# Optimization experiments

Hardware: AMD Instinct MI355X
Metric: run time of the kernel (lower is better)

## Reference

```python
import jax, jax.numpy as jnp
import numpy as np

N, C, O, H, S, SHARE = 30000, 128, 128, 8, 16, 8
D = O // H            # mid_planes = 16
OS = O // SHARE       # 16
OFFSETS = [15000, 30000]
EPS = 1e-5


def _knn(p, offsets, k):
    """Exact per-batch KNN (incl. self), chunked to bound memory."""
    n = p.shape[0]
    idx = np.empty((n, k), dtype=np.int64)
    start = 0
    for end in offsets:
        pb = p[start:end]
        sq = (pb * pb).sum(-1)
        for qs in range(0, pb.shape[0], 1024):
            q = pb[qs:qs + 1024]
            d = sq[qs:qs + q.shape[0], None] - 2.0 * (q @ pb.T) + sq[None, :]
            part = np.argpartition(d, k - 1, axis=1)[:, :k]
            idx[start + qs:start + qs + q.shape[0]] = part + start
        start = end
    return idx


def _ln(x, g, b):
    m = x.mean(-1, keepdims=True)
    v = ((x - m) ** 2).mean(-1, keepdims=True)
    return (x - m) / jnp.sqrt(v + EPS) * g + b


def setup_inputs() -> dict:
    rng = np.random.default_rng(0)
    p_np = (rng.standard_normal((N, 3)) * 5.0).astype(np.float32)
    idx = _knn(p_np, OFFSETS, S)

    key = jax.random.key(0)
    ks = jax.random.split(key, 12)

    def lin(k, i, o):
        return (jax.random.normal(k, (i, o), jnp.float32) / np.sqrt(i)).astype(jnp.float32)

    return {
        "p": jnp.asarray(p_np),
        "x": jax.random.normal(ks[0], (N, C), jnp.float32),
        "idx": jnp.asarray(idx),
        "Wq": lin(ks[1], C, O), "bq": jnp.zeros((O,), jnp.float32),
        "Wk": lin(ks[2], C, O), "bk": jnp.zeros((O,), jnp.float32),
        "Wv": lin(ks[3], C, O), "bv": jnp.zeros((O,), jnp.float32),
        "Wp1": lin(ks[4], 3, 3), "bp1": jnp.zeros((3,), jnp.float32),
        "gp": jnp.ones((3,), jnp.float32), "betap": jnp.zeros((3,), jnp.float32),
        "Wp2": lin(ks[5], 3, O), "bp2": jnp.zeros((O,), jnp.float32),
        "gw1": jnp.ones((D,), jnp.float32), "betaw1": jnp.zeros((D,), jnp.float32),
        "Ww1": lin(ks[6], D, OS), "bw1": jnp.zeros((OS,), jnp.float32),
        "gw2": jnp.ones((OS,), jnp.float32), "betaw2": jnp.zeros((OS,), jnp.float32),
        "Ww2": lin(ks[7], OS, OS), "bw2": jnp.zeros((OS,), jnp.float32),
    }


def reference(p, x, idx, Wq, bq, Wk, bk, Wv, bv, Wp1, bp1, gp, betap, Wp2, bp2,
              gw1, betaw1, Ww1, bw1, gw2, betaw2, Ww2, bw2):
    xq = (x @ Wq + bq).reshape(N, H, D)          # (N,H,D)
    xk = x @ Wk + bk                              # (N,O)
    xv = x @ Wv + bv
    kg = xk[idx].reshape(N, S, H, D)              # neighbor gather
    vg = xv[idx].reshape(N, S, H, D)
    pr = p[idx] - p[:, None, :]                   # relative coords (N,S,3)
    pe = jax.nn.relu(_ln(pr @ Wp1 + bp1, gp, betap)) @ Wp2 + bp2  # (N,S,O)
    pe = pe.reshape(N, S, H, D)
    r = kg + pe - xq[:, None]                     # (N,S,H,D)
    w = jax.nn.relu(_ln(r, gw1, betaw1)) @ Ww1 + bw1
    w = jax.nn.relu(_ln(w, gw2, betaw2)) @ Ww2 + bw2  # (N,S,H,OS)
    w = jax.nn.softmax(w.mean(-1), axis=1)        # softmax over the S neighbors
    out = ((vg + pe) * w[..., None]).sum(axis=1)  # weighted neighbor reduce
    return out.reshape(N, O)
```

## Files before the change

### kernel.cpp

```cpp
#include <hip/hip_runtime.h>
#include <math.h>

typedef unsigned int  uint;
typedef unsigned short ushort;

constexpr int NPTS = 30000;
constexpr int NPAD = 30080;
constexpr int CIN  = 128;
constexpr int OC   = 128;
constexpr int NH   = 8;
constexpr int NS   = 16;
constexpr int DH   = 16;
constexpr int OSH  = 16;
constexpr float EPSF = 1e-5f;

typedef __attribute__((ext_vector_type(8))) short bf16x8;
typedef __attribute__((ext_vector_type(4))) float f32x4;
typedef __attribute__((ext_vector_type(2))) __fp16 h16x2;

__device__ __forceinline__ ushort f2bf(float f) {
    uint u = __float_as_uint(f);
    u += 0x7fff + ((u >> 16) & 1);
    return (ushort)(u >> 16);
}
__device__ __forceinline__ void bf2f2(uint u, float& f0, float& f1) {
    f0 = __uint_as_float(u << 16);
    f1 = __uint_as_float(u & 0xffff0000u);
}

#if defined(__has_builtin)
#if __has_builtin(__builtin_amdgcn_fdot2)
#define HAVE_FDOT2 1
#endif
#endif

constexpr int XB_BLOCKS = (NPAD * CIN / 4) / 256;

__global__ __launch_bounds__(256) void prep_kernel(
    const float* __restrict__ x,
    const float* __restrict__ Wq, const float* __restrict__ Wk, const float* __restrict__ Wv,
    const float* __restrict__ Ww1, const float* __restrict__ Ww2, const float* __restrict__ bw2,
    ushort* __restrict__ xb, ushort* __restrict__ WT,
    uint* __restrict__ Ww1p, float* __restrict__ rmean)
{
    const int b = blockIdx.x;
    const int t = threadIdx.x;
    if (b < XB_BLOCKS) {
        int e   = (b * 256 + t) * 4;
        int row = e >> 7;
        uint2 o = make_uint2(0, 0);
        if (row < NPTS) {
            float4 f = *(const float4*)(x + e);
            o.x = (uint)f2bf(f.x) | ((uint)f2bf(f.y) << 16);
            o.y = (uint)f2bf(f.z) | ((uint)f2bf(f.w) << 16);
        }
        *(uint2*)(xb + e) = o;
    } else if (b < XB_BLOCKS + 3) {
        int mat = b - XB_BLOCKS;
        const float* W = (mat == 0) ? Wq : (mat == 1 ? Wk : Wv);
        ushort* T = WT + mat * OC * CIN;
        if (t < OC) {
            for (int k = 0; k < CIN; ++k)
                T[t * CIN + k] = f2bf(W[k * OC + t]);
        }
    } else {
        if (t < 128) {
            int d2 = t >> 4, o2 = t & 15;
            h16x2 pk = __builtin_amdgcn_cvt_pkrtz(Ww1[(2 * d2) * OSH + o2],
                                                  Ww1[(2 * d2 + 1) * OSH + o2]);
            Ww1p[t] = *(uint*)&pk;
        } else if (t >= 128 && t < 144) {
            int d = t - 128;
            float acc = 0.f;
            #pragma unroll
            for (int o2 = 0; o2 < OSH; ++o2) acc += Ww2[d * OSH + o2];
            rmean[d] = acc * (1.f / OSH);
        } else if (t == 144) {
            float acc = 0.f;
            #pragma unroll
            for (int o2 = 0; o2 < OSH; ++o2) acc += bw2[o2];
            rmean[OSH] = acc * (1.f / OSH);
        }
    }
}

__global__ __launch_bounds__(256) void qkv_mfma(
    const ushort* __restrict__ xb, const ushort* __restrict__ WT,
    const float* __restrict__ bq, const float* __restrict__ bk, const float* __restrict__ bv,
    ushort* __restrict__ yq, ushort* __restrict__ yk, ushort* __restrict__ yv)
{
    const int mat = blockIdx.y;
    const float* bias = (mat == 0) ? bq : (mat == 1 ? bk : bv);
    ushort* y         = (mat == 0) ? yq : (mat == 1 ? yk : yv);
    const ushort* T   = WT + mat * OC * CIN;

    const int n0   = blockIdx.x * 128;
    const int t    = threadIdx.x;
    const int wave = t >> 6;
    const int lane = t & 63;
    const int m16  = lane & 15;
    const int quad = lane >> 4;

    f32x4 acc[2][8];
    #pragma unroll
    for (int mt = 0; mt < 2; ++mt)
        #pragma unroll
        for (int nt = 0; nt < 8; ++nt)
            acc[mt][nt] = (f32x4){0.f, 0.f, 0.f, 0.f};

    const ushort* arow0 = xb + (size_t)(n0 + wave * 32 + m16) * CIN;
    const ushort* arow1 = arow0 + 16 * CIN;

    #pragma unroll
    for (int ks = 0; ks < 4; ++ks) {
        const int kb = ks * 32 + quad * 8;
        bf16x8 a0 = *(const bf16x8*)(arow0 + kb);
        bf16x8 a1 = *(const bf16x8*)(arow1 + kb);
        #pragma unroll
        for (int nt = 0; nt < 8; ++nt) {
            bf16x8 bfr = *(const bf16x8*)(T + (size_t)(nt * 16 + m16) * CIN + kb);
            acc[0][nt] = __builtin_amdgcn_mfma_f32_16x16x32_bf16(a0, bfr, acc[0][nt], 0, 0, 0);
            acc[1][nt] = __builtin_amdgcn_mfma_f32_16x16x32_bf16(a1, bfr, acc[1][nt], 0, 0, 0);
        }
    }

    #pragma unroll
    for (int mt = 0; mt < 2; ++mt) {
        #pragma unroll
        for (int nt = 0; nt < 8; ++nt) {
            const int col = nt * 16 + m16;
            const float bcol = bias[col];
            #pragma unroll
            for (int r = 0; r < 4; ++r) {
                int row = n0 + wave * 32 + mt * 16 + quad * 4 + r;
                if (row < NPTS)
                    y[(size_t)row * OC + col] = f2bf(acc[mt][nt][r] + bcol);
            }
        }
    }
}

__global__ __launch_bounds__(128) void attn_kernel(
    const float* __restrict__ p, const int* __restrict__ idx,
    const ushort* __restrict__ xq, const ushort* __restrict__ xk, const ushort* __restrict__ xv,
    const float* __restrict__ Wp1, const float* __restrict__ bp1,
    const float* __restrict__ gp,  const float* __restrict__ betap,
    const float* __restrict__ Wp2, const float* __restrict__ bp2,
    const float* __restrict__ gw1, const float* __restrict__ betaw1,
    const float* __restrict__ Ww1, const float* __restrict__ bw1,
    const float* __restrict__ gw2, const float* __restrict__ betaw2,
    const uint* __restrict__ Ww1p, const float* __restrict__ rmean,
    float* __restrict__ out)
{
    const int n = blockIdx.x;
    const int t = threadIdx.x;
    const int s = t >> 3;
    const int h = t & 7;

    __shared__ float s_t[NS][4];
    __shared__ float s_logit[NS][NH];
    __shared__ float s_mx[NH];
    __shared__ float s_inv[NH];
    __shared__ float s_contrib[NS][OC + 4];

    if (t < NS) {
        int ss = t;
        int j = idx[n * NS + ss];
        float pr0 = p[j * 3 + 0] - p[n * 3 + 0];
        float pr1 = p[j * 3 + 1] - p[n * 3 + 1];
        float pr2 = p[j * 3 + 2] - p[n * 3 + 2];
        float u[3];
        #pragma unroll
        for (int c = 0; c < 3; ++c)
            u[c] = bp1[c] + pr0 * Wp1[0 * 3 + c] + pr1 * Wp1[1 * 3 + c] + pr2 * Wp1[2 * 3 + c];
        float m   = (u[0] + u[1] + u[2]) * (1.f / 3.f);
        float d0 = u[0] - m, d1 = u[1] - m, d2 = u[2] - m;
        float var = (d0 * d0 + d1 * d1 + d2 * d2) * (1.f / 3.f);
        float inv = rsqrtf(var + EPSF);
        #pragma unroll
        for (int c = 0; c < 3; ++c)
            s_t[ss][c] = fmaxf((u[c] - m) * inv * gp[c] + betap[c], 0.f);
    }
    __syncthreads();

    const int j = idx[n * NS + s];
    const float t0 = s_t[s][0], t1 = s_t[s][1], t2 = s_t[s][2];
    const int obase = h * DH;

    float pe[DH];
    {
        const float* W0 = Wp2 + obase;
        const float* W1 = Wp2 + OC + obase;
        const float* W2 = Wp2 + 2 * OC + obase;
        const float* B  = bp2 + obase;
        #pragma unroll
        for (int q = 0; q < 4; ++q) {
            float4 a0 = *(const float4*)(W0 + q * 4);
            float4 a1 = *(const float4*)(W1 + q * 4);
            float4 a2 = *(const float4*)(W2 + q * 4);
            float4 bb = *(const float4*)(B + q * 4);
            pe[q * 4 + 0] = bb.x + t0 * a0.x + t1 * a1.x + t2 * a2.x;
            pe[q * 4 + 1] = bb.y + t0 * a0.y + t1 * a1.y + t2 * a2.y;
            pe[q * 4 + 2] = bb.z + t0 * a0.z + t1 * a1.z + t2 * a2.z;
            pe[q * 4 + 3] = bb.w + t0 * a0.w + t1 * a1.w + t2 * a2.w;
        }
    }

    float vv[DH], r[DH];
    {
        const uint4* k4 = (const uint4*)(xk + (size_t)j * OC + obase);
        const uint4* v4 = (const uint4*)(xv + (size_t)j * OC + obase);
        const uint4* q4 = (const uint4*)(xq + (size_t)n * OC + obase);
        uint4 ku0 = k4[0], ku1 = k4[1];
        uint4 vu0 = v4[0], vu1 = v4[1];
        uint4 qu0 = q4[0], qu1 = q4[1];
        float kf[DH], qf[DH];
        bf2f2(ku0.x, kf[0], kf[1]);   bf2f2(ku0.y, kf[2], kf[3]);
        bf2f2(ku0.z, kf[4], kf[5]);   bf2f2(ku0.w, kf[6], kf[7]);
        bf2f2(ku1.x, kf[8], kf[9]);   bf2f2(ku1.y, kf[10], kf[11]);
        bf2f2(ku1.z, kf[12], kf[13]); bf2f2(ku1.w, kf[14], kf[15]);
        bf2f2(vu0.x, vv[0], vv[1]);   bf2f2(vu0.y, vv[2], vv[3]);
        bf2f2(vu0.z, vv[4], vv[5]);   bf2f2(vu0.w, vv[6], vv[7]);
        bf2f2(vu1.x, vv[8], vv[9]);   bf2f2(vu1.y, vv[10], vv[11]);
        bf2f2(vu1.z, vv[12], vv[13]); bf2f2(vu1.w, vv[14], vv[15]);
        bf2f2(qu0.x, qf[0], qf[1]);   bf2f2(qu0.y, qf[2], qf[3]);
        bf2f2(qu0.z, qf[4], qf[5]);   bf2f2(qu0.w, qf[6], qf[7]);
        bf2f2(qu1.x, qf[8], qf[9]);   bf2f2(qu1.y, qf[10], qf[11]);
        bf2f2(qu1.z, qf[12], qf[13]); bf2f2(qu1.w, qf[14], qf[15]);
        #pragma unroll
        for (int d = 0; d < DH; ++d)
            r[d] = kf[d] + pe[d] - qf[d];
    }

    float a[DH];
    {
        float m = 0.f;
        #pragma unroll
        for (int d = 0; d < DH; ++d) m += r[d];
        m *= (1.f / DH);
        float var = 0.f;
        #pragma unroll
        for (int d = 0; d < DH; ++d) { float dd = r[d] - m; var += dd * dd; }
        var *= (1.f / DH);
        float inv = rsqrtf(var + EPSF);
        #pragma unroll
        for (int d = 0; d < DH; ++d)
            a[d] = fmaxf((r[d] - m) * inv * gw1[d] + betaw1[d], 0.f);
    }

    float w1[OSH];
    #pragma unroll
    for (int o2 = 0; o2 < OSH; ++o2) w1[o2] = bw1[o2];
#ifdef HAVE_FDOT2
    {
        h16x2 ap[8];
        #pragma unroll
        for (int d2 = 0; d2 < 8; ++d2)
            ap[d2] = __builtin_amdgcn_cvt_pkrtz(a[2 * d2], a[2 * d2 + 1]);
        #pragma unroll
        for (int d2 = 0; d2 < 8; ++d2) {
            #pragma unroll
            for (int o2 = 0; o2 < OSH; ++o2) {
                uint wp = Ww1p[d2 * OSH + o2];
                w1[o2] = __builtin_amdgcn_fdot2(ap[d2], *(h16x2*)&wp, w1[o2], false);
            }
        }
    }
#else
    #pragma unroll
    for (int d = 0; d < DH; ++d) {
        float av = a[d];
        #pragma unroll
        for (int o2 = 0; o2 < OSH; ++o2) w1[o2] = fmaf(av, Ww1[d * OSH + o2], w1[o2]);
    }
#endif

    float logit;
    {
        float m = 0.f;
        #pragma unroll
        for (int o2 = 0; o2 < OSH; ++o2) m += w1[o2];
        m *= (1.f / OSH);
        float var = 0.f;
        #pragma unroll
        for (int o2 = 0; o2 < OSH; ++o2) { float dd = w1[o2] - m; var += dd * dd; }
        var *= (1.f / OSH);
        float inv = rsqrtf(var + EPSF);
        logit = rmean[OSH];
        #pragma unroll
        for (int o2 = 0; o2 < OSH; ++o2) {
            float bv2 = fmaxf((w1[o2] - m) * inv * gw2[o2] + betaw2[o2], 0.f);
            logit = fmaf(bv2, rmean[o2], logit);
        }
    }

    s_logit[s][h] = logit;
    __syncthreads();

    if (t < NH) {
        float mx = -1e30f;
        #pragma unroll
        for (int ss = 0; ss < NS; ++ss) mx = fmaxf(mx, s_logit[ss][t]);
        float denom = 0.f;
        #pragma unroll
        for (int ss = 0; ss < NS; ++ss) denom += __expf(s_logit[ss][t] - mx);
        s_mx[t] = mx;
        s_inv[t] = 1.f / denom;
    }
    __syncthreads();

    float w = __expf(logit - s_mx[h]) * s_inv[h];

    #pragma unroll
    for (int d = 0; d < DH; ++d)
        s_contrib[s][obase + d] = (vv[d] + pe[d]) * w;
    __syncthreads();

    float acc = 0.f;
    #pragma unroll
    for (int ss = 0; ss < NS; ++ss) acc += s_contrib[ss][t];
    out[(size_t)n * OC + t] = acc;
}

extern "C" void kernel_launch(void* const* d_in, const int* in_sizes, int n_in,
                              void* d_out, int out_size, void* d_ws, size_t ws_size,
                              hipStream_t stream) {
    const float* p     = (const float*)d_in[0];
    const float* x     = (const float*)d_in[1];
    const int*   idx   = (const int*)d_in[2];
    const float* Wq    = (const float*)d_in[3];
    const float* bq    = (const float*)d_in[4];
    const float* Wk    = (const float*)d_in[5];
    const float* bk    = (const float*)d_in[6];
    const float* Wv    = (const float*)d_in[7];
    const float* bv    = (const float*)d_in[8];
    const float* Wp1   = (const float*)d_in[9];
    const float* bp1   = (const float*)d_in[10];
    const float* gp    = (const float*)d_in[11];
    const float* betap = (const float*)d_in[12];
    const float* Wp2   = (const float*)d_in[13];
    const float* bp2   = (const float*)d_in[14];
    const float* gw1   = (const float*)d_in[15];
    const float* betaw1= (const float*)d_in[16];
    const float* Ww1   = (const float*)d_in[17];
    const float* bw1   = (const float*)d_in[18];
    const float* gw2   = (const float*)d_in[19];
    const float* betaw2= (const float*)d_in[20];
    const float* Ww2   = (const float*)d_in[21];
    const float* bw2   = (const float*)d_in[22];
    float* out = (float*)d_out;

    ushort* xb = (ushort*)d_ws;
    ushort* WT = xb + (size_t)NPAD * CIN;
    ushort* xq = WT + 3 * OC * CIN;
    ushort* xk = xq + (size_t)NPTS * OC;
    ushort* xv = xk + (size_t)NPTS * OC;
    uint*   Ww1p  = (uint*)(xv + (size_t)NPTS * OC);
    float*  rmean = (float*)(Ww1p + 128);

    prep_kernel<<<XB_BLOCKS + 4, 256, 0, stream>>>(x, Wq, Wk, Wv, Ww1, Ww2, bw2,
                                                   xb, WT, Ww1p, rmean);

    dim3 g1(NPAD / 128, 3);
    qkv_mfma<<<g1, 256, 0, stream>>>(xb, WT, bq, bk, bv, xq, xk, xv);

    attn_kernel<<<NPTS, 128, 0, stream>>>(p, idx, xq, xk, xv,
                                          Wp1, bp1, gp, betap, Wp2, bp2,
                                          gw1, betaw1, Ww1, bw1,
                                          gw2, betaw2, Ww1p, rmean, out);
}
```

Before: 223.3 us.

## Switch attention math to packed fp16 with prepacked half-precision parameters

New measurement: 196.2 us. 12.1% less time.

```diff
diff --git a/kernel.cpp b/kernel.cpp
--- a/kernel.cpp
+++ b/kernel.cpp
@@ -14,34 +14,58 @@
 constexpr int OSH  = 16;
 constexpr float EPSF = 1e-5f;
 
-typedef __attribute__((ext_vector_type(8))) short bf16x8;
-typedef __attribute__((ext_vector_type(4))) float f32x4;
-typedef __attribute__((ext_vector_type(2))) __fp16 h16x2;
+typedef __attribute__((ext_vector_type(8))) short  bf16x8;
+typedef __attribute__((ext_vector_type(4))) float  f32x4;
+typedef __attribute__((ext_vector_type(2))) __fp16 h2;
 
 __device__ __forceinline__ ushort f2bf(float f) {
     uint u = __float_as_uint(f);
     u += 0x7fff + ((u >> 16) & 1);
     return (ushort)(u >> 16);
 }
-__device__ __forceinline__ void bf2f2(uint u, float& f0, float& f1) {
-    f0 = __uint_as_float(u << 16);
-    f1 = __uint_as_float(u & 0xffff0000u);
-}
+__device__ __forceinline__ ushort f2h(float f) {
+    __fp16 h = (__fp16)f;
+    return *(ushort*)&h;
+}
+__device__ __forceinline__ uint pk2(float a, float b) {
+    h2 v = __builtin_amdgcn_cvt_pkrtz(a, b);
+    return *(uint*)&v;
+}
+__device__ __forceinline__ h2 asH2(uint u) { return *(h2*)&u; }
 
 #if defined(__has_builtin)
-#if __has_builtin(__builtin_amdgcn_fdot2)
-#define HAVE_FDOT2 1
+#if __has_builtin(__builtin_elementwise_max)
+#define PKMAX(a, b) __builtin_elementwise_max(a, b)
 #endif
 #endif
+#ifndef PKMAX
+__device__ __forceinline__ h2 PKMAX(h2 a, h2 b) {
+    h2 r; r[0] = a[0] > b[0] ? a[0] : b[0]; r[1] = a[1] > b[1] ? a[1] : b[1]; return r;
+}
+#endif
+
+constexpr int PK_WW1   = 0;
+constexpr int PK_WP2   = 128;
+constexpr int PK_BP2   = 320;
+constexpr int PK_GW1   = 384;
+constexpr int PK_BW1P  = 392;
+constexpr int PK_GW2   = 400;
+constexpr int PK_BW2P  = 408;
+constexpr int PK_RM    = 416;
+constexpr int PKF_BW1  = 424;
+constexpr int PKF_RMB  = 440;
 
 constexpr int XB_BLOCKS = (NPAD * CIN / 4) / 256;
 
 __global__ __launch_bounds__(256) void prep_kernel(
     const float* __restrict__ x,
     const float* __restrict__ Wq, const float* __restrict__ Wk, const float* __restrict__ Wv,
-    const float* __restrict__ Ww1, const float* __restrict__ Ww2, const float* __restrict__ bw2,
-    ushort* __restrict__ xb, ushort* __restrict__ WT,
-    uint* __restrict__ Ww1p, float* __restrict__ rmean)
+    const float* __restrict__ Wp2, const float* __restrict__ bp2,
+    const float* __restrict__ gw1, const float* __restrict__ betaw1,
+    const float* __restrict__ Ww1, const float* __restrict__ bw1,
+    const float* __restrict__ gw2, const float* __restrict__ betaw2,
+    const float* __restrict__ Ww2, const float* __restrict__ bw2,
+    ushort* __restrict__ xb, ushort* __restrict__ WT, uint* __restrict__ PK)
 {
     const int b = blockIdx.x;
     const int t = threadIdx.x;
@@ -64,22 +88,37 @@
                 T[t * CIN + k] = f2bf(W[k * OC + t]);
         }
     } else {
+        float* FPK = (float*)PK;
         if (t < 128) {
-            int d2 = t >> 4, o2 = t & 15;
-            h16x2 pk = __builtin_amdgcn_cvt_pkrtz(Ww1[(2 * d2) * OSH + o2],
-                                                  Ww1[(2 * d2 + 1) * OSH + o2]);
-            Ww1p[t] = *(uint*)&pk;
-        } else if (t >= 128 && t < 144) {
-            int d = t - 128;
-            float acc = 0.f;
+            int dp = t >> 4, o = t & 15;
+            PK[PK_WW1 + t] = pk2(Ww1[(2 * dp) * OSH + o], Ww1[(2 * dp + 1) * OSH + o]);
+        }
+        if (t < 192) {
+            int c = t >> 6, jj = t & 63;
+            PK[PK_WP2 + t] = pk2(Wp2[c * OC + 2 * jj], Wp2[c * OC + 2 * jj + 1]);
+        }
+        if (t < 64)
+            PK[PK_BP2 + t] = pk2(bp2[2 * t], bp2[2 * t + 1]);
+        if (t < 8) {
+            PK[PK_GW1 + t]  = pk2(gw1[2 * t],    gw1[2 * t + 1]);
+            PK[PK_BW1P + t] = pk2(betaw1[2 * t], betaw1[2 * t + 1]);
+            PK[PK_GW2 + t]  = pk2(gw2[2 * t],    gw2[2 * t + 1]);
+            PK[PK_BW2P + t] = pk2(betaw2[2 * t], betaw2[2 * t + 1]);
+            float r0 = 0.f, r1 = 0.f;
             #pragma unroll
-            for (int o2 = 0; o2 < OSH; ++o2) acc += Ww2[d * OSH + o2];
-            rmean[d] = acc * (1.f / OSH);
-        } else if (t == 144) {
+            for (int o2 = 0; o2 < OSH; ++o2) {
+                r0 += Ww2[(2 * t) * OSH + o2];
+                r1 += Ww2[(2 * t + 1) * OSH + o2];
+            }
+            PK[PK_RM + t] = pk2(r0 * (1.f / OSH), r1 * (1.f / OSH));
+        }
+        if (t < 16)
+            FPK[PKF_BW1 + t] = bw1[t];
+        if (t == 16) {
             float acc = 0.f;
             #pragma unroll
             for (int o2 = 0; o2 < OSH; ++o2) acc += bw2[o2];
-            rmean[OSH] = acc * (1.f / OSH);
+            FPK[PKF_RMB] = acc * (1.f / OSH);
         }
     }
 }
@@ -134,7 +173,7 @@
             for (int r = 0; r < 4; ++r) {
                 int row = n0 + wave * 32 + mt * 16 + quad * 4 + r;
                 if (row < NPTS)
-                    y[(size_t)row * OC + col] = f2bf(acc[mt][nt][r] + bcol);
+                    y[(size_t)row * OC + col] = f2h(acc[mt][nt][r] + bcol);
             }
         }
     }
@@ -145,11 +184,7 @@
     const ushort* __restrict__ xq, const ushort* __restrict__ xk, const ushort* __restrict__ xv,
     const float* __restrict__ Wp1, const float* __restrict__ bp1,
     const float* __restrict__ gp,  const float* __restrict__ betap,
-    const float* __restrict__ Wp2, const float* __restrict__ bp2,
-    const float* __restrict__ gw1, const float* __restrict__ betaw1,
-    const float* __restrict__ Ww1, const float* __restrict__ bw1,
-    const float* __restrict__ gw2, const float* __restrict__ betaw2,
-    const uint* __restrict__ Ww1p, const float* __restrict__ rmean,
+    const uint* __restrict__ PK,
     float* __restrict__ out)
 {
     const int n = blockIdx.x;
@@ -157,11 +192,13 @@
     const int s = t >> 3;
     const int h = t & 7;
 
+    const float* FPK = (const float*)PK;
+
     __shared__ float s_t[NS][4];
     __shared__ float s_logit[NS][NH];
     __shared__ float s_mx[NH];
     __shared__ float s_inv[NH];
-    __shared__ float s_contrib[NS][OC + 4];
+    __shared__ uint  s_c[NS][68];
 
     if (t < NS) {
         int ss = t;
@@ -187,110 +224,99 @@
     const float t0 = s_t[s][0], t1 = s_t[s][1], t2 = s_t[s][2];
     const int obase = h * DH;
 
-    float pe[DH];
-    {
-        const float* W0 = Wp2 + obase;
-        const float* W1 = Wp2 + OC + obase;
-        const float* W2 = Wp2 + 2 * OC + obase;
-        const float* B  = bp2 + obase;
-        #pragma unroll
-        for (int q = 0; q < 4; ++q) {
-            float4 a0 = *(const float4*)(W0 + q * 4);
-            float4 a1 = *(const float4*)(W1 + q * 4);
-            float4 a2 = *(const float4*)(W2 + q * 4);
-            float4 bb = *(const float4*)(B + q * 4);
-            pe[q * 4 + 0] = bb.x + t0 * a0.x + t1 * a1.x + t2 * a2.x;
-            pe[q * 4 + 1] = bb.y + t0 * a0.y + t1 * a1.y + t2 * a2.y;
-            pe[q * 4 + 2] = bb.z + t0 * a0.z + t1 * a1.z + t2 * a2.z;
-            pe[q * 4 + 3] = bb.w + t0 * a0.w + t1 * a1.w + t2 * a2.w;
-        }
-    }
-
-    float vv[DH], r[DH];
-    {
+    __attribute__((aligned(16))) h2 pe2[8];
+    {
+        h2 t02 = asH2(pk2(t0, t0));
+        h2 t12 = asH2(pk2(t1, t1));
+        h2 t22 = asH2(pk2(t2, t2));
+        const uint* W0p = PK + PK_WP2 + 0 * 64 + h * 8;
+        const uint* W1p = PK + PK_WP2 + 1 * 64 + h * 8;
+        const uint* W2p = PK + PK_WP2 + 2 * 64 + h * 8;
+        const uint* Bp  = PK + PK_BP2 + h * 8;
+        #pragma unroll
+        for (int i = 0; i < 8; ++i) {
+            h2 acc = asH2(Bp[i]);
+            acc = acc + t02 * asH2(W0p[i]);
+            acc = acc + t12 * asH2(W1p[i]);
+            acc = acc + t22 * asH2(W2p[i]);
+            pe2[i] = acc;
+        }
+    }
+
+    __attribute__((aligned(16))) h2 v2[8], r2[8];
+    {
+        __attribute__((aligned(16))) h2 k2[8], q2[8];
         const uint4* k4 = (const uint4*)(xk + (size_t)j * OC + obase);
         const uint4* v4 = (const uint4*)(xv + (size_t)j * OC + obase);
         const uint4* q4 = (const uint4*)(xq + (size_t)n * OC + obase);
-        uint4 ku0 = k4[0], ku1 = k4[1];
-        uint4 vu0 = v4[0], vu1 = v4[1];
-        uint4 qu0 = q4[0], qu1 = q4[1];
-        float kf[DH], qf[DH];
-        bf2f2(ku0.x, kf[0], kf[1]);   bf2f2(ku0.y, kf[2], kf[3]);
-        bf2f2(ku0.z, kf[4], kf[5]);   bf2f2(ku0.w, kf[6], kf[7]);
-        bf2f2(ku1.x, kf[8], kf[9]);   bf2f2(ku1.y, kf[10], kf[11]);
-        bf2f2(ku1.z, kf[12], kf[13]); bf2f2(ku1.w, kf[14], kf[15]);
-        bf2f2(vu0.x, vv[0], vv[1]);   bf2f2(vu0.y, vv[2], vv[3]);
-        bf2f2(vu0.z, vv[4], vv[5]);   bf2f2(vu0.w, vv[6], vv[7]);
-        bf2f2(vu1.x, vv[8], vv[9]);   bf2f2(vu1.y, vv[10], vv[11]);
-        bf2f2(vu1.z, vv[12], vv[13]); bf2f2(vu1.w, vv[14], vv[15]);
-        bf2f2(qu0.x, qf[0], qf[1]);   bf2f2(qu0.y, qf[2], qf[3]);
-        bf2f2(qu0.z, qf[4], qf[5]);   bf2f2(qu0.w, qf[6], qf[7]);
-        bf2f2(qu1.x, qf[8], qf[9]);   bf2f2(qu1.y, qf[10], qf[11]);
-        bf2f2(qu1.z, qf[12], qf[13]); bf2f2(qu1.w, qf[14], qf[15]);
-        #pragma unroll
-        for (int d = 0; d < DH; ++d)
-            r[d] = kf[d] + pe[d] - qf[d];
-    }
-
-    float a[DH];
-    {
-        float m = 0.f;
-        #pragma unroll
-        for (int d = 0; d < DH; ++d) m += r[d];
-        m *= (1.f / DH);
-        float var = 0.f;
-        #pragma unroll
-        for (int d = 0; d < DH; ++d) { float dd = r[d] - m; var += dd * dd; }
-        var *= (1.f / DH);
+        *(uint4*)&k2[0] = k4[0]; *(uint4*)&k2[4] = k4[1];
+        *(uint4*)&v2[0] = v4[0]; *(uint4*)&v2[4] = v4[1];
+        *(uint4*)&q2[0] = q4[0]; *(uint4*)&q2[4] = q4[1];
+        #pragma unroll
+        for (int i = 0; i < 8; ++i)
+            r2[i] = (k2[i] + pe2[i]) - q2[i];
+    }
+
+    __attribute__((aligned(16))) h2 a2[8];
+    {
+        h2 sum2 = r2[0];
+        #pragma unroll
+        for (int i = 1; i < 8; ++i) sum2 = sum2 + r2[i];
+        float m = ((float)sum2[0] + (float)sum2[1]) * (1.f / DH);
+        h2 m2 = asH2(pk2(m, m));
+        h2 vs2 = {(__fp16)0.f, (__fp16)0.f};
+        #pragma unroll
+        for (int i = 0; i < 8; ++i) {
+            r2[i] = r2[i] - m2;
+            vs2 = vs2 + r2[i] * r2[i];
+        }
+        float var = ((float)vs2[0] + (float)vs2[1]) * (1.f / DH);
         float inv = rsqrtf(var + EPSF);
-        #pragma unroll
-        for (int d = 0; d < DH; ++d)
-            a[d] = fmaxf((r[d] - m) * inv * gw1[d] + betaw1[d], 0.f);
+        h2 inv2 = asH2(pk2(inv, inv));
+        h2 z2 = {(__fp16)0.f, (__fp16)0.f};
+        #pragma unroll
+        for (int i = 0; i < 8; ++i) {
+            h2 gi = asH2(PK[PK_GW1 + i]) * inv2;
+            a2[i] = PKMAX(r2[i] * gi + asH2(PK[PK_BW1P + i]), z2);
+        }
     }
 
     float w1[OSH];
     #pragma unroll
-    for (int o2 = 0; o2 < OSH; ++o2) w1[o2] = bw1[o2];
-#ifdef HAVE_FDOT2
-    {
-        h16x2 ap[8];
-        #pragma unroll
-        for (int d2 = 0; d2 < 8; ++d2)
-            ap[d2] = __builtin_amdgcn_cvt_pkrtz(a[2 * d2], a[2 * d2 + 1]);
-        #pragma unroll
-        for (int d2 = 0; d2 < 8; ++d2) {
-            #pragma unroll
-            for (int o2 = 0; o2 < OSH; ++o2) {
-                uint wp = Ww1p[d2 * OSH + o2];
-                w1[o2] = __builtin_amdgcn_fdot2(ap[d2], *(h16x2*)&wp, w1[o2], false);
-            }
-        }
-    }
-#else
+    for (int o2 = 0; o2 < OSH; ++o2) w1[o2] = FPK[PKF_BW1 + o2];
     #pragma unroll
-    for (int d = 0; d < DH; ++d) {
-        float av = a[d];
-        #pragma unroll
-        for (int o2 = 0; o2 < OSH; ++o2) w1[o2] = fmaf(av, Ww1[d * OSH + o2], w1[o2]);
-    }
-#endif
+    for (int dp = 0; dp < 8; ++dp) {
+        #pragma unroll
+        for (int o2 = 0; o2 < OSH; ++o2)
+            w1[o2] = __builtin_amdgcn_fdot2(a2[dp], asH2(PK[PK_WW1 + dp * 16 + o2]), w1[o2], false);
+    }
 
     float logit;
     {
-        float m = 0.f;
-        #pragma unroll
-        for (int o2 = 0; o2 < OSH; ++o2) m += w1[o2];
-        m *= (1.f / OSH);
-        float var = 0.f;
-        #pragma unroll
-        for (int o2 = 0; o2 < OSH; ++o2) { float dd = w1[o2] - m; var += dd * dd; }
-        var *= (1.f / OSH);
+        __attribute__((aligned(16))) h2 w2[8];
+        #pragma unroll
+        for (int i = 0; i < 8; ++i) w2[i] = asH2(pk2(w1[2 * i], w1[2 * i + 1]));
+        h2 sum2 = w2[0];
+        #pragma unroll
+        for (int i = 1; i < 8; ++i) sum2 = sum2 + w2[i];
+        float m = ((float)sum2[0] + (float)sum2[1]) * (1.f / OSH);
+        h2 m2 = asH2(pk2(m, m));
+        h2 vs2 = {(__fp16)0.f, (__fp16)0.f};
+        #pragma unroll
+        for (int i = 0; i < 8; ++i) {
+            w2[i] = w2[i] - m2;
+            vs2 = vs2 + w2[i] * w2[i];
+        }
+        float var = ((float)vs2[0] + (float)vs2[1]) * (1.f / OSH);
         float inv = rsqrtf(var + EPSF);
-        logit = rmean[OSH];
-        #pragma unroll
-        for (int o2 = 0; o2 < OSH; ++o2) {
-            float bv2 = fmaxf((w1[o2] - m) * inv * gw2[o2] + betaw2[o2], 0.f);
-            logit = fmaf(bv2, rmean[o2], logit);
+        h2 inv2 = asH2(pk2(inv, inv));
+        h2 z2 = {(__fp16)0.f, (__fp16)0.f};
+        logit = FPK[PKF_RMB];
+        #pragma unroll
+        for (int i = 0; i < 8; ++i) {
+            h2 gi = asH2(PK[PK_GW2 + i]) * inv2;
+            h2 bv2 = PKMAX(w2[i] * gi + asH2(PK[PK_BW2P + i]), z2);
+            logit = __builtin_amdgcn_fdot2(bv2, asH2(PK[PK_RM + i]), logit, false);
         }
     }
 
@@ -311,15 +337,27 @@
 
     float w = __expf(logit - s_mx[h]) * s_inv[h];
 
-    #pragma unroll
-    for (int d = 0; d < DH; ++d)
-        s_contrib[s][obase + d] = (vv[d] + pe[d]) * w;
+    {
+        h2 w2p = asH2(pk2(w, w));
+        __attribute__((aligned(16))) h2 c2[8];
+        #pragma unroll
+        for (int i = 0; i < 8; ++i)
+            c2[i] = (v2[i] + pe2[i]) * w2p;
+        *(uint4*)&s_c[s][h * 8]     = *(uint4*)&c2[0];
+        *(uint4*)&s_c[s][h * 8 + 4] = *(uint4*)&c2[4];
+    }
     __syncthreads();
 
-    float acc = 0.f;
-    #pragma unroll
-    for (int ss = 0; ss < NS; ++ss) acc += s_contrib[ss][t];
-    out[(size_t)n * OC + t] = acc;
+    {
+        const int oh = t >> 4;
+        const int od = t & 15;
+        const int col = oh * 8 + (od >> 1);
+        h2 acc2 = {(__fp16)0.f, (__fp16)0.f};
+        #pragma unroll
+        for (int ss = 0; ss < NS; ++ss)
+            acc2 = acc2 + asH2(s_c[ss][col]);
+        out[(size_t)n * OC + t] = (float)acc2[od & 1];
+    }
 }
 
 extern "C" void kernel_launch(void* const* d_in, const int* in_sizes, int n_in,
@@ -355,17 +393,17 @@
     ushort* xq = WT + 3 * OC * CIN;
     ushort* xk = xq + (size_t)NPTS * OC;
     ushort* xv = xk + (size_t)NPTS * OC;
-    uint*   Ww1p  = (uint*)(xv + (size_t)NPTS * OC);
-    float*  rmean = (float*)(Ww1p + 128);
-
-    prep_kernel<<<XB_BLOCKS + 4, 256, 0, stream>>>(x, Wq, Wk, Wv, Ww1, Ww2, bw2,
-                                                   xb, WT, Ww1p, rmean);
+    uint*   PACKS = (uint*)(xv + (size_t)NPTS * OC);
+
+    prep_kernel<<<XB_BLOCKS + 4, 256, 0, stream>>>(x, Wq, Wk, Wv,
+                                                   Wp2, bp2, gw1, betaw1,
+                                                   Ww1, bw1, gw2, betaw2, Ww2, bw2,
+                                                   xb, WT, PACKS);
 
     dim3 g1(NPAD / 128, 3);
     qkv_mfma<<<g1, 256, 0, stream>>>(xb, WT, bq, bk, bv, xq, xk, xv);
 
     attn_kernel<<<NPTS, 128, 0, stream>>>(p, idx, xq, xk, xv,
-                                          Wp1, bp1, gp, betap, Wp2, bp2,
-                                          gw1, betaw1, Ww1, bw1,
-                                          gw2, betaw2, Ww1p, rmean, out);
-}
+                                          Wp1, bp1, gp, betap,
+                                          PACKS, out);
+}
```
